# Kernel tuning notes

Hardware: AMD Instinct MI355X
Metric: run time of the kernel (lower is better)

The kernel has to match this reference:

```python
import jax, jax.numpy as jnp
import numpy as np

N_NODES = 10000


def gcn_conv(x, W, b, src, dst, n):
    # GCNConv (PyG defaults): linear transform, add self-loops, symmetric norm,
    # scatter-add aggregation at target nodes, then bias.
    h = x @ W  # [n, out]
    # degree with self-loops: 1 (self) + count of incoming edges per target node
    deg = jnp.ones((n,), h.dtype).at[dst].add(1.0)
    dinv = jax.lax.rsqrt(deg)  # deg >= 1 always
    norm = dinv[src] * dinv[dst]  # [E]
    # edge messages + self-loop contribution (norm_ii = dinv_i^2)
    agg = jnp.zeros_like(h).at[dst].add(h[src] * norm[:, None])
    agg = agg + h * (dinv * dinv)[:, None]
    return agg + b


def setup_inputs() -> dict:
    key = jax.random.key(0)
    ks = jax.random.split(key, 8)
    d_in, d_hid, d_out = 512, 512, 100
    n, e = N_NODES, 160000
    x = jax.random.normal(ks[0], (n, d_in), dtype=jnp.float32)
    edge_index = jax.random.randint(ks[1], (2, e), 0, n, dtype=jnp.int64)
    s1 = 1.0 / np.sqrt(d_in)
    s2 = 1.0 / np.sqrt(d_hid)
    W1 = jax.random.uniform(ks[2], (d_in, d_hid), jnp.float32, -s1, s1)
    b1 = jnp.zeros((d_hid,), jnp.float32)
    W2 = jax.random.uniform(ks[3], (d_hid, d_hid), jnp.float32, -s2, s2)
    b2 = jnp.zeros((d_hid,), jnp.float32)
    Wc = jax.random.uniform(ks[4], (d_hid, d_out), jnp.float32, -s2, s2)
    bc = jax.random.uniform(ks[5], (d_out,), jnp.float32, -s2, s2)
    return {"x": x, "edge_index": edge_index, "W1": W1, "b1": b1,
            "W2": W2, "b2": b2, "Wc": Wc, "bc": bc}


def reference(x, edge_index, W1, b1, W2, b2, Wc, bc):
    src, dst = edge_index[0], edge_index[1]
    n = x.shape[0]
    h = gcn_conv(x, W1, b1, src, dst, n)
    h = jax.nn.relu(h)  # dropout is identity in eval mode
    h = gcn_conv(h, W2, b2, src, dst, n)
    return h @ Wc + bc
```

## Files before the change

### kernel.cpp

```cpp
#include <hip/hip_runtime.h>
#include <hip/hip_bf16.h>
#include <stdint.h>

typedef __bf16 bf16_t;
typedef bf16_t bf16x8 __attribute__((ext_vector_type(8)));
typedef float f32x4 __attribute__((ext_vector_type(4)));

#define NN 10000
#define ELLCAP 64

__device__ __forceinline__ float b2f(unsigned short u) {
  union { unsigned int i; float f; } c; c.i = ((unsigned int)u) << 16; return c.f;
}
__device__ __forceinline__ unsigned short f2b(float f) {
  union { float f; unsigned int i; } c; c.f = f;
  unsigned int x = c.i;
  x += 0x7FFFu + ((x >> 16) & 1u);
  return (unsigned short)(x >> 16);
}
__device__ __forceinline__ uint4 cvt8(float4 a, float4 b) {
  uint4 r;
  r.x = (unsigned int)f2b(a.x) | ((unsigned int)f2b(a.y) << 16);
  r.y = (unsigned int)f2b(a.z) | ((unsigned int)f2b(a.w) << 16);
  r.z = (unsigned int)f2b(b.x) | ((unsigned int)f2b(b.y) << 16);
  r.w = (unsigned int)f2b(b.z) | ((unsigned int)f2b(b.w) << 16);
  return r;
}
__device__ __forceinline__ void load_lds16(const void* g, void* l) {
  __builtin_amdgcn_global_load_lds(
      (const __attribute__((address_space(1))) unsigned int*)g,
      (__attribute__((address_space(3))) unsigned int*)l, 16, 0, 0);
}
__device__ __forceinline__ f32x4 mfma16(bf16x8 a, bf16x8 b, f32x4 c) {
  return __builtin_amdgcn_mfma_f32_16x16x32_bf16(a, b, c, 0, 0, 0);
}

template <bool OBF16>
__device__ void gemm64(const unsigned short* __restrict__ A, const unsigned short* __restrict__ Bt,
                       void* __restrict__ Cv, int M, int Ncols, int ldc, int tm, int tn,
                       unsigned short* __restrict__ As, unsigned short* __restrict__ Bs)
{
  const int tid = threadIdx.x;
  const int lane = tid & 63;
  const int wn = tid >> 6;
  const int quad = lane >> 4, l15 = lane & 15;

  const int r0 = tid >> 2, kc = tid & 3;
  int ga = tm * 64 + r0;  if (ga > M - 1) ga = M - 1;
  const int gb0 = tn * 128 + r0;
  const int gb1 = tn * 128 + 64 + r0;
  const unsigned short* gA  = A + (size_t)ga * 512 + kc * 8;
  const unsigned short* gB0 = Bt + (size_t)gb0 * 512 + kc * 8;
  const unsigned short* gB1 = Bt + (size_t)gb1 * 512 + kc * 8;
  const int loff  = r0 * 32 + kc * 8;
  const int loff1 = (64 + r0) * 32 + kc * 8;
  const int ABUF = 64 * 32, BBUF = 128 * 32;

  f32x4 acc[4][2];
  #pragma unroll
  for (int i = 0; i < 4; i++)
    #pragma unroll
    for (int j = 0; j < 2; j++) {
      f32x4 z = {0.f, 0.f, 0.f, 0.f};
      acc[i][j] = z;
    }

  load_lds16(gA,  &As[loff]);
  load_lds16(gB0, &Bs[loff]);
  load_lds16(gB1, &Bs[loff1]);
  __syncthreads();

  for (int it = 0; it < 16; ++it) {
    const int ca = (it & 1) * ABUF, cb = (it & 1) * BBUF;
    if (it < 15) {
      const int k1 = (it + 1) * 32;
      const int na = ((it & 1) ^ 1) * ABUF, nb = ((it & 1) ^ 1) * BBUF;
      load_lds16(gA + k1,  &As[na + loff]);
      load_lds16(gB0 + k1, &Bs[nb + loff]);
      load_lds16(gB1 + k1, &Bs[nb + loff1]);
    }
    bf16x8 af[4], bfr[2];
    #pragma unroll
    for (int i = 0; i < 4; i++)
      af[i] = *(const bf16x8*)&As[ca + (i * 16 + l15) * 32 + quad * 8];
    #pragma unroll
    for (int j = 0; j < 2; j++)
      bfr[j] = *(const bf16x8*)&Bs[cb + (wn * 32 + j * 16 + l15) * 32 + quad * 8];
    #pragma unroll
    for (int i = 0; i < 4; i++)
      #pragma unroll
      for (int j = 0; j < 2; j++)
        acc[i][j] = mfma16(af[i], bfr[j], acc[i][j]);
    __syncthreads();
  }

  #pragma unroll
  for (int i = 0; i < 4; i++) {
    const int row_base = tm * 64 + i * 16 + quad * 4;
    #pragma unroll
    for (int j = 0; j < 2; j++) {
      const int col = tn * 128 + wn * 32 + j * 16 + l15;
      if (col < Ncols) {
        #pragma unroll
        for (int r = 0; r < 4; r++) {
          int row = row_base + r;
          if (row < M) {
            float v = acc[i][j][r];
            if (OBF16) ((unsigned short*)Cv)[(size_t)row * ldc + col] = f2b(v);
            else       ((float*)Cv)[(size_t)row * ldc + col] = v;
          }
        }
      }
    }
  }
}

__device__ void gemm64_f32A(const float* __restrict__ A, const unsigned short* __restrict__ Bt,
                            unsigned short* __restrict__ C, int M, int tm, int tn,
                            unsigned short* __restrict__ As, unsigned short* __restrict__ Bs)
{
  const int tid = threadIdx.x;
  const int lane = tid & 63;
  const int wn = tid >> 6;
  const int quad = lane >> 4, l15 = lane & 15;

  const int r0 = tid >> 2, kc = tid & 3;
  int ga = tm * 64 + r0;  if (ga > M - 1) ga = M - 1;
  const int gb0 = tn * 128 + r0;
  const int gb1 = tn * 128 + 64 + r0;
  const float* gA = A + (size_t)ga * 512 + kc * 8;
  const unsigned short* gB0 = Bt + (size_t)gb0 * 512 + kc * 8;
  const unsigned short* gB1 = Bt + (size_t)gb1 * 512 + kc * 8;
  const int loff  = r0 * 32 + kc * 8;
  const int loff1 = (64 + r0) * 32 + kc * 8;
  const int ABUF = 64 * 32, BBUF = 128 * 32;

  f32x4 acc[4][2];
  #pragma unroll
  for (int i = 0; i < 4; i++)
    #pragma unroll
    for (int j = 0; j < 2; j++) {
      f32x4 z = {0.f, 0.f, 0.f, 0.f};
      acc[i][j] = z;
    }

  {
    float4 a0 = *(const float4*)(gA), a1 = *(const float4*)(gA + 4);
    *(uint4*)&As[loff] = cvt8(a0, a1);
    load_lds16(gB0, &Bs[loff]);
    load_lds16(gB1, &Bs[loff1]);
  }
  __syncthreads();

  for (int it = 0; it < 16; ++it) {
    const int ca = (it & 1) * ABUF, cb = (it & 1) * BBUF;
    const int na = ((it & 1) ^ 1) * ABUF, nb = ((it & 1) ^ 1) * BBUF;
    float4 a0, a1;
    if (it < 15) {
      const int k1 = (it + 1) * 32;
      a0 = *(const float4*)(gA + k1);  a1 = *(const float4*)(gA + k1 + 4);
      load_lds16(gB0 + k1, &Bs[nb + loff]);
      load_lds16(gB1 + k1, &Bs[nb + loff1]);
    }
    bf16x8 af[4], bfr[2];
    #pragma unroll
    for (int i = 0; i < 4; i++)
      af[i] = *(const bf16x8*)&As[ca + (i * 16 + l15) * 32 + quad * 8];
    #pragma unroll
    for (int j = 0; j < 2; j++)
      bfr[j] = *(const bf16x8*)&Bs[cb + (wn * 32 + j * 16 + l15) * 32 + quad * 8];
    #pragma unroll
    for (int i = 0; i < 4; i++)
      #pragma unroll
      for (int j = 0; j < 2; j++)
        acc[i][j] = mfma16(af[i], bfr[j], acc[i][j]);
    if (it < 15) *(uint4*)&As[na + loff] = cvt8(a0, a1);
    __syncthreads();
  }

  #pragma unroll
  for (int i = 0; i < 4; i++) {
    const int row_base = tm * 64 + i * 16 + quad * 4;
    #pragma unroll
    for (int j = 0; j < 2; j++) {
      const int col = tn * 128 + wn * 32 + j * 16 + l15;
      #pragma unroll
      for (int r = 0; r < 4; r++) {
        int row = row_base + r;
        if (row < M) C[(size_t)row * 512 + col] = f2b(acc[i][j][r]);
      }
    }
  }
}

__device__ void wtrans_tile(const float* __restrict__ W, unsigned short* __restrict__ Wt,
                            int ncols, int tr0, int tc0)
{
  __shared__ float tile[64][65];
  const int t = threadIdx.x;
  const int r = t >> 2, c4 = t & 3;
  #pragma unroll
  for (int i = 0; i < 4; i++) {
    int col = c4 * 16 + i * 4;
    int gc = tc0 + col;
    float4 v;
    if (gc + 3 < ncols) {
      v = *(const float4*)&W[(size_t)(tr0 + r) * ncols + gc];
    } else {
      v.x = (gc + 0 < ncols) ? W[(size_t)(tr0 + r) * ncols + gc + 0] : 0.f;
      v.y = (gc + 1 < ncols) ? W[(size_t)(tr0 + r) * ncols + gc + 1] : 0.f;
      v.z = (gc + 2 < ncols) ? W[(size_t)(tr0 + r) * ncols + gc + 2] : 0.f;
      v.w = (gc + 3 < ncols) ? W[(size_t)(tr0 + r) * ncols + gc + 3] : 0.f;
    }
    tile[r][col] = v.x; tile[r][col + 1] = v.y;
    tile[r][col + 2] = v.z; tile[r][col + 3] = v.w;
  }
  __syncthreads();
  const int o = t >> 2;
  #pragma unroll
  for (int i = 0; i < 4; i++) {
    int k = c4 * 16 + i * 4;
    ushort4 u;
    u.x = f2b(tile[k + 0][o]); u.y = f2b(tile[k + 1][o]);
    u.z = f2b(tile[k + 2][o]); u.w = f2b(tile[k + 3][o]);
    *(ushort4*)&Wt[(size_t)(tc0 + o) * 512 + tr0 + k] = u;
  }
}

__global__ __launch_bounds__(256)
void prep_fill(const float* __restrict__ W1, const float* __restrict__ Wc,
               const float* __restrict__ W2, const int* __restrict__ src,
               const int* __restrict__ dst, int* __restrict__ cnt,
               int* __restrict__ ell, unsigned short* __restrict__ W1t,
               unsigned short* __restrict__ Wct, unsigned short* __restrict__ w2b, int E)
{
  if (blockIdx.x < 64) { wtrans_tile(W1, W1t, 512, (blockIdx.x >> 3) * 64, (blockIdx.x & 7) * 64); return; }
  if (blockIdx.x < 80) { int b = blockIdx.x - 64; wtrans_tile(Wc, Wct, 100, (b >> 1) * 64, (b & 1) * 64); return; }
  const int t0 = (blockIdx.x - 80) * 256 + threadIdx.x;
  const int FT = 160 * 256;
  const float4* W24 = (const float4*)W2;
  uint4* w2b4 = (uint4*)w2b;
  for (int i = t0; i < 512 * 512 / 8; i += FT)
    w2b4[i] = cvt8(W24[i * 2], W24[i * 2 + 1]);
  for (int e = t0; e < E; e += FT) {
    int s = src[e], d = dst[e];
    int pos = atomicAdd(&cnt[d], 1);
    if (pos < ELLCAP) ell[d * ELLCAP + pos] = s;
  }
}

__global__ __launch_bounds__(256)
void gemm1_fold(const float* __restrict__ x, const unsigned short* __restrict__ W1t,
                unsigned short* __restrict__ B2,
                const unsigned short* __restrict__ Wct, const unsigned short* __restrict__ w2b,
                unsigned short* __restrict__ W2WcT,
                const float* __restrict__ b2, const float* __restrict__ Wc,
                const float* __restrict__ bc, float* __restrict__ bias2c)
{
  __shared__ __align__(16) unsigned short As[2 * 64 * 32];
  __shared__ __align__(16) unsigned short Bs[2 * 128 * 32];
  const int b = blockIdx.x;
  if (b < 628) {
    gemm64_f32A(x, W1t, B2, NN, b >> 2, b & 3, As, Bs);
  } else if (b < 636) {
    const int g = b - 628;
    gemm64<true>(Wct, w2b, W2WcT, 128, 512, 512, g >> 2, g & 3, As, Bs);
  } else {
    const int j = threadIdx.x;
    if (j < 128) {
      float s = 0.f;
      if (j < 100) {
        s = bc[j];
        for (int k = 0; k < 512; k++) s = fmaf(b2[k], Wc[k * 100 + j], s);
      }
      bias2c[j] = s;
    }
  }
}

__device__ __forceinline__ void acc8(float* a, uint4 v, float nm) {
  a[0] = fmaf(b2f((unsigned short)(v.x & 0xffffu)), nm, a[0]);
  a[1] = fmaf(b2f((unsigned short)(v.x >> 16)),     nm, a[1]);
  a[2] = fmaf(b2f((unsigned short)(v.y & 0xffffu)), nm, a[2]);
  a[3] = fmaf(b2f((unsigned short)(v.y >> 16)),     nm, a[3]);
  a[4] = fmaf(b2f((unsigned short)(v.z & 0xffffu)), nm, a[4]);
  a[5] = fmaf(b2f((unsigned short)(v.z >> 16)),     nm, a[5]);
  a[6] = fmaf(b2f((unsigned short)(v.w & 0xffffu)), nm, a[6]);
  a[7] = fmaf(b2f((unsigned short)(v.w >> 16)),     nm, a[7]);
}

__global__ __launch_bounds__(256)
void gather1(const unsigned short* __restrict__ h, const int* __restrict__ cnt,
             const int* __restrict__ ell, const float* __restrict__ bias,
             unsigned short* __restrict__ outb, int n)
{
  int node = blockIdx.x * 4 + (threadIdx.x >> 6);
  if (node >= n) return;
  const int lane = threadIdx.x & 63;
  const int c8 = lane * 8;

  int cd = cnt[node]; if (cd > ELLCAP) cd = ELLCAP;
  const float fd = (float)(1 + cd);
  const float slf = 1.0f / fd;
  uint4 hv = *(const uint4*)&h[(size_t)node * 512 + c8];
  const float4* bp = (const float4*)&bias[c8];
  float4 b0 = bp[0], b1 = bp[1];
  float a[8] = {b0.x, b0.y, b0.z, b0.w, b1.x, b1.y, b1.z, b1.w};
  acc8(a, hv, slf);

  const int* row = ell + node * ELLCAP;
  int j = 0;
  for (; j + 8 <= cd; j += 8) {
    int ss[8]; uint4 vv[8]; float nm[8];
    #pragma unroll
    for (int q = 0; q < 8; q++) ss[q] = row[j + q];
    #pragma unroll
    for (int q = 0; q < 8; q++) vv[q] = *(const uint4*)&h[(size_t)ss[q] * 512 + c8];
    #pragma unroll
    for (int q = 0; q < 8; q++) nm[q] = rsqrtf((float)(1 + cnt[ss[q]]) * fd);
    #pragma unroll
    for (int q = 0; q < 8; q++) acc8(a, vv[q], nm[q]);
  }
  for (; j < cd; ++j) {
    int s = row[j];
    uint4 v = *(const uint4*)&h[(size_t)s * 512 + c8];
    acc8(a, v, rsqrtf((float)(1 + cnt[s]) * fd));
  }
  #pragma unroll
  for (int q = 0; q < 8; q++) a[q] = fmaxf(a[q], 0.f);
  uint4 o;
  o.x = (unsigned int)f2b(a[0]) | ((unsigned int)f2b(a[1]) << 16);
  o.y = (unsigned int)f2b(a[2]) | ((unsigned int)f2b(a[3]) << 16);
  o.z = (unsigned int)f2b(a[4]) | ((unsigned int)f2b(a[5]) << 16);
  o.w = (unsigned int)f2b(a[6]) | ((unsigned int)f2b(a[7]) << 16);
  *(uint4*)&outb[(size_t)node * 512 + c8] = o;
}

__global__ __launch_bounds__(256)
void gemm2c(const unsigned short* __restrict__ B1, const unsigned short* __restrict__ W2WcT,
            unsigned short* __restrict__ Z)
{
  __shared__ __align__(16) unsigned short As[2 * 64 * 32];
  __shared__ __align__(16) unsigned short Bs[2 * 128 * 32];
  gemm64<true>(B1, W2WcT, Z, NN, 128, 128, blockIdx.x, 0, As, Bs);
}

__global__ __launch_bounds__(256)
void gather2c(const unsigned short* __restrict__ Z, const int* __restrict__ cnt,
              const int* __restrict__ ell, const float* __restrict__ bias2c,
              float* __restrict__ out, int n)
{
  int node = blockIdx.x * 4 + (threadIdx.x >> 6);
  if (node >= n) return;
  const int lane = threadIdx.x & 63;
  const int c2 = lane * 2;
  const float2 bb = *(const float2*)&bias2c[c2];

  int cd = cnt[node]; if (cd > ELLCAP) cd = ELLCAP;
  const float fd = (float)(1 + cd);
  const float slf = 1.0f / fd;
  unsigned int hv = *(const unsigned int*)&Z[(size_t)node * 128 + c2];
  float a0 = fmaf(b2f((unsigned short)(hv & 0xffffu)), slf, bb.x);
  float a1 = fmaf(b2f((unsigned short)(hv >> 16)),     slf, bb.y);

  const int* row = ell + node * ELLCAP;
  int j = 0;
  for (; j + 8 <= cd; j += 8) {
    int ss[8]; unsigned int vv[8]; float nm[8];
    #pragma unroll
    for (int q = 0; q < 8; q++) ss[q] = row[j + q];
    #pragma unroll
    for (int q = 0; q < 8; q++) vv[q] = *(const unsigned int*)&Z[(size_t)ss[q] * 128 + c2];
    #pragma unroll
    for (int q = 0; q < 8; q++) nm[q] = rsqrtf((float)(1 + cnt[ss[q]]) * fd);
    #pragma unroll
    for (int q = 0; q < 8; q++) {
      a0 = fmaf(b2f((unsigned short)(vv[q] & 0xffffu)), nm[q], a0);
      a1 = fmaf(b2f((unsigned short)(vv[q] >> 16)),     nm[q], a1);
    }
  }
  for (; j < cd; ++j) {
    int s = row[j];
    unsigned int v = *(const unsigned int*)&Z[(size_t)s * 128 + c2];
    float nm = rsqrtf((float)(1 + cnt[s]) * fd);
    a0 = fmaf(b2f((unsigned short)(v & 0xffffu)), nm, a0);
    a1 = fmaf(b2f((unsigned short)(v >> 16)),     nm, a1);
  }
  if (c2 < 100)
    *(float2*)&out[(size_t)node * 100 + c2] = make_float2(a0, a1);
}

extern "C" void kernel_launch(void* const* d_in, const int* in_sizes, int n_in,
                              void* d_out, int out_size, void* d_ws, size_t ws_size,
                              hipStream_t stream) {
  const float* x  = (const float*)d_in[0];
  const int*   ei = (const int*)d_in[1];
  const float* W1 = (const float*)d_in[2];
  const float* b1 = (const float*)d_in[3];
  const float* W2 = (const float*)d_in[4];
  const float* b2 = (const float*)d_in[5];
  const float* Wc = (const float*)d_in[6];
  const float* bc = (const float*)d_in[7];
  float* out = (float*)d_out;

  const int n = NN;
  const int E = in_sizes[1] / 2;
  const int* src = ei;
  const int* dst = ei + E;

  char* w = (char*)d_ws;
  int* cnt = (int*)w;                       w += ((n * 4 + 255) / 256) * 256;
  int* ell = (int*)w;                       w += ((n * ELLCAP * 4 + 255) / 256) * 256;
  float* bias2c = (float*)w;                w += 512;
  unsigned short* W1t = (unsigned short*)w; w += 512 * 512 * 2;
  unsigned short* Wct = (unsigned short*)w; w += 128 * 512 * 2;
  unsigned short* w2b = (unsigned short*)w; w += 512 * 512 * 2;
  unsigned short* W2WcT = (unsigned short*)w; w += 128 * 512 * 2;
  unsigned short* B1  = (unsigned short*)w; w += (size_t)n * 512 * 2;
  unsigned short* B2  = (unsigned short*)w; w += (size_t)n * 512 * 2;
  unsigned short* Z   = (unsigned short*)w; w += (size_t)n * 128 * 2;

  const int nb_g = (n + 3) / 4;

  hipMemsetAsync(cnt, 0, n * sizeof(int), stream);
  prep_fill<<<240, 256, 0, stream>>>(W1, Wc, W2, src, dst, cnt, ell, W1t, Wct, w2b, E);
  gemm1_fold<<<637, 256, 0, stream>>>(x, W1t, B2, Wct, w2b, W2WcT, b2, Wc, bc, bias2c);
  gather1<<<nb_g, 256, 0, stream>>>(B2, cnt, ell, b1, B1, n);
  gemm2c<<<157, 256, 0, stream>>>(B1, W2WcT, Z);
  gather2c<<<nb_g, 256, 0, stream>>>(Z, cnt, ell, bias2c, out, n);
}
```

Measured before the change: 157.4 us.

## Fold source-side degree norm into GEMM epilogues and pre-convert x to bf16

The GEMM epilogues now scale each output row by rsqrt(1+deg), so the gathers only sum neighbour rows and apply the destination dinv and bias at the end. This removes the per-edge cnt lookups and rsqrt calls from both gather kernels. Separately, x is converted to bf16 in prep_fill (stored in the B1 buffer), so the first GEMM uses the plain bf16 path with global-to-LDS loads. The cost is an extra full pass that writes x as bf16, and the first GEMM now depends on cnt being complete before it runs.

Measured after the change: 159.1 us. About the same (+1.1%).

```diff
diff --git a/kernel.cpp b/kernel.cpp
--- a/kernel.cpp
+++ b/kernel.cpp
@@ -35,9 +35,10 @@
   return __builtin_amdgcn_mfma_f32_16x16x32_bf16(a, b, c, 0, 0, 0);
 }
 
-template <bool OBF16>
+template <bool SCALED>
 __device__ void gemm64(const unsigned short* __restrict__ A, const unsigned short* __restrict__ Bt,
-                       void* __restrict__ Cv, int M, int Ncols, int ldc, int tm, int tn,
+                       unsigned short* __restrict__ C, const int* __restrict__ cntp,
+                       int M, int Ncols, int ldc, int tm, int tn,
                        unsigned short* __restrict__ As, unsigned short* __restrict__ Bs)
 {
   const int tid = threadIdx.x;
@@ -96,98 +97,21 @@
 
   #pragma unroll
   for (int i = 0; i < 4; i++) {
-    const int row_base = tm * 64 + i * 16 + quad * 4;
-    #pragma unroll
-    for (int j = 0; j < 2; j++) {
-      const int col = tn * 128 + wn * 32 + j * 16 + l15;
-      if (col < Ncols) {
+    #pragma unroll
+    for (int r = 0; r < 4; r++) {
+      const int row = tm * 64 + i * 16 + quad * 4 + r;
+      if (row < M) {
+        float dv = 1.f;
+        if (SCALED) {
+          int c = cntp[row]; if (c > ELLCAP) c = ELLCAP;
+          dv = rsqrtf((float)(1 + c));
+        }
         #pragma unroll
-        for (int r = 0; r < 4; r++) {
-          int row = row_base + r;
-          if (row < M) {
-            float v = acc[i][j][r];
-            if (OBF16) ((unsigned short*)Cv)[(size_t)row * ldc + col] = f2b(v);
-            else       ((float*)Cv)[(size_t)row * ldc + col] = v;
-          }
+        for (int j = 0; j < 2; j++) {
+          const int col = tn * 128 + wn * 32 + j * 16 + l15;
+          if (col < Ncols)
+            C[(size_t)row * ldc + col] = f2b(acc[i][j][r] * dv);
         }
-      }
-    }
-  }
-}
-
-__device__ void gemm64_f32A(const float* __restrict__ A, const unsigned short* __restrict__ Bt,
-                            unsigned short* __restrict__ C, int M, int tm, int tn,
-                            unsigned short* __restrict__ As, unsigned short* __restrict__ Bs)
-{
-  const int tid = threadIdx.x;
-  const int lane = tid & 63;
-  const int wn = tid >> 6;
-  const int quad = lane >> 4, l15 = lane & 15;
-
-  const int r0 = tid >> 2, kc = tid & 3;
-  int ga = tm * 64 + r0;  if (ga > M - 1) ga = M - 1;
-  const int gb0 = tn * 128 + r0;
-  const int gb1 = tn * 128 + 64 + r0;
-  const float* gA = A + (size_t)ga * 512 + kc * 8;
-  const unsigned short* gB0 = Bt + (size_t)gb0 * 512 + kc * 8;
-  const unsigned short* gB1 = Bt + (size_t)gb1 * 512 + kc * 8;
-  const int loff  = r0 * 32 + kc * 8;
-  const int loff1 = (64 + r0) * 32 + kc * 8;
-  const int ABUF = 64 * 32, BBUF = 128 * 32;
-
-  f32x4 acc[4][2];
-  #pragma unroll
-  for (int i = 0; i < 4; i++)
-    #pragma unroll
-    for (int j = 0; j < 2; j++) {
-      f32x4 z = {0.f, 0.f, 0.f, 0.f};
-      acc[i][j] = z;
-    }
-
-  {
-    float4 a0 = *(const float4*)(gA), a1 = *(const float4*)(gA + 4);
-    *(uint4*)&As[loff] = cvt8(a0, a1);
-    load_lds16(gB0, &Bs[loff]);
-    load_lds16(gB1, &Bs[loff1]);
-  }
-  __syncthreads();
-
-  for (int it = 0; it < 16; ++it) {
-    const int ca = (it & 1) * ABUF, cb = (it & 1) * BBUF;
-    const int na = ((it & 1) ^ 1) * ABUF, nb = ((it & 1) ^ 1) * BBUF;
-    float4 a0, a1;
-    if (it < 15) {
-      const int k1 = (it + 1) * 32;
-      a0 = *(const float4*)(gA + k1);  a1 = *(const float4*)(gA + k1 + 4);
-      load_lds16(gB0 + k1, &Bs[nb + loff]);
-      load_lds16(gB1 + k1, &Bs[nb + loff1]);
-    }
-    bf16x8 af[4], bfr[2];
-    #pragma unroll
-    for (int i = 0; i < 4; i++)
-      af[i] = *(const bf16x8*)&As[ca + (i * 16 + l15) * 32 + quad * 8];
-    #pragma unroll
-    for (int j = 0; j < 2; j++)
-      bfr[j] = *(const bf16x8*)&Bs[cb + (wn * 32 + j * 16 + l15) * 32 + quad * 8];
-    #pragma unroll
-    for (int i = 0; i < 4; i++)
-      #pragma unroll
-      for (int j = 0; j < 2; j++)
-        acc[i][j] = mfma16(af[i], bfr[j], acc[i][j]);
-    if (it < 15) *(uint4*)&As[na + loff] = cvt8(a0, a1);
-    __syncthreads();
-  }
-
-  #pragma unroll
-  for (int i = 0; i < 4; i++) {
-    const int row_base = tm * 64 + i * 16 + quad * 4;
-    #pragma unroll
-    for (int j = 0; j < 2; j++) {
-      const int col = tn * 128 + wn * 32 + j * 16 + l15;
-      #pragma unroll
-      for (int r = 0; r < 4; r++) {
-        int row = row_base + r;
-        if (row < M) C[(size_t)row * 512 + col] = f2b(acc[i][j][r]);
       }
     }
   }
@@ -229,19 +153,24 @@
 
 __global__ __launch_bounds__(256)
 void prep_fill(const float* __restrict__ W1, const float* __restrict__ Wc,
-               const float* __restrict__ W2, const int* __restrict__ src,
-               const int* __restrict__ dst, int* __restrict__ cnt,
-               int* __restrict__ ell, unsigned short* __restrict__ W1t,
-               unsigned short* __restrict__ Wct, unsigned short* __restrict__ w2b, int E)
+               const float* __restrict__ W2, const float* __restrict__ x,
+               const int* __restrict__ src, const int* __restrict__ dst,
+               int* __restrict__ cnt, int* __restrict__ ell,
+               unsigned short* __restrict__ W1t, unsigned short* __restrict__ Wct,
+               unsigned short* __restrict__ w2b, unsigned short* __restrict__ xb, int E)
 {
   if (blockIdx.x < 64) { wtrans_tile(W1, W1t, 512, (blockIdx.x >> 3) * 64, (blockIdx.x & 7) * 64); return; }
   if (blockIdx.x < 80) { int b = blockIdx.x - 64; wtrans_tile(Wc, Wct, 100, (b >> 1) * 64, (b & 1) * 64); return; }
   const int t0 = (blockIdx.x - 80) * 256 + threadIdx.x;
-  const int FT = 160 * 256;
+  const int FT = 256 * 256;
   const float4* W24 = (const float4*)W2;
   uint4* w2b4 = (uint4*)w2b;
   for (int i = t0; i < 512 * 512 / 8; i += FT)
     w2b4[i] = cvt8(W24[i * 2], W24[i * 2 + 1]);
+  const float4* x4 = (const float4*)x;
+  uint4* xb4 = (uint4*)xb;
+  for (int i = t0; i < NN * 512 / 8; i += FT)
+    xb4[i] = cvt8(x4[i * 2], x4[i * 2 + 1]);
   for (int e = t0; e < E; e += FT) {
     int s = src[e], d = dst[e];
     int pos = atomicAdd(&cnt[d], 1);
@@ -250,8 +179,8 @@
 }
 
 __global__ __launch_bounds__(256)
-void gemm1_fold(const float* __restrict__ x, const unsigned short* __restrict__ W1t,
-                unsigned short* __restrict__ B2,
+void gemm1_fold(const unsigned short* __restrict__ xb, const unsigned short* __restrict__ W1t,
+                unsigned short* __restrict__ B2, const int* __restrict__ cnt,
                 const unsigned short* __restrict__ Wct, const unsigned short* __restrict__ w2b,
                 unsigned short* __restrict__ W2WcT,
                 const float* __restrict__ b2, const float* __restrict__ Wc,
@@ -261,10 +190,10 @@
   __shared__ __align__(16) unsigned short Bs[2 * 128 * 32];
   const int b = blockIdx.x;
   if (b < 628) {
-    gemm64_f32A(x, W1t, B2, NN, b >> 2, b & 3, As, Bs);
+    gemm64<true>(xb, W1t, B2, cnt, NN, 512, 512, b >> 2, b & 3, As, Bs);
   } else if (b < 636) {
     const int g = b - 628;
-    gemm64<true>(Wct, w2b, W2WcT, 128, 512, 512, g >> 2, g & 3, As, Bs);
+    gemm64<false>(Wct, w2b, W2WcT, nullptr, 128, 512, 512, g >> 2, g & 3, As, Bs);
   } else {
     const int j = threadIdx.x;
     if (j < 128) {
@@ -278,15 +207,15 @@
   }
 }
 
-__device__ __forceinline__ void acc8(float* a, uint4 v, float nm) {
-  a[0] = fmaf(b2f((unsigned short)(v.x & 0xffffu)), nm, a[0]);
-  a[1] = fmaf(b2f((unsigned short)(v.x >> 16)),     nm, a[1]);
-  a[2] = fmaf(b2f((unsigned short)(v.y & 0xffffu)), nm, a[2]);
-  a[3] = fmaf(b2f((unsigned short)(v.y >> 16)),     nm, a[3]);
-  a[4] = fmaf(b2f((unsigned short)(v.z & 0xffffu)), nm, a[4]);
-  a[5] = fmaf(b2f((unsigned short)(v.z >> 16)),     nm, a[5]);
-  a[6] = fmaf(b2f((unsigned short)(v.w & 0xffffu)), nm, a[6]);
-  a[7] = fmaf(b2f((unsigned short)(v.w >> 16)),     nm, a[7]);
+__device__ __forceinline__ void add8(float* a, uint4 v) {
+  a[0] += b2f((unsigned short)(v.x & 0xffffu));
+  a[1] += b2f((unsigned short)(v.x >> 16));
+  a[2] += b2f((unsigned short)(v.y & 0xffffu));
+  a[3] += b2f((unsigned short)(v.y >> 16));
+  a[4] += b2f((unsigned short)(v.z & 0xffffu));
+  a[5] += b2f((unsigned short)(v.z >> 16));
+  a[6] += b2f((unsigned short)(v.w & 0xffffu));
+  a[7] += b2f((unsigned short)(v.w >> 16));
 }
 
 __global__ __launch_bounds__(256)
@@ -300,34 +229,33 @@
   const int c8 = lane * 8;
 
   int cd = cnt[node]; if (cd > ELLCAP) cd = ELLCAP;
-  const float fd = (float)(1 + cd);
-  const float slf = 1.0f / fd;
+  const float dinv = rsqrtf((float)(1 + cd));
   uint4 hv = *(const uint4*)&h[(size_t)node * 512 + c8];
-  const float4* bp = (const float4*)&bias[c8];
-  float4 b0 = bp[0], b1 = bp[1];
-  float a[8] = {b0.x, b0.y, b0.z, b0.w, b1.x, b1.y, b1.z, b1.w};
-  acc8(a, hv, slf);
+  float a[8] = {0.f, 0.f, 0.f, 0.f, 0.f, 0.f, 0.f, 0.f};
+  add8(a, hv);
 
   const int* row = ell + node * ELLCAP;
   int j = 0;
   for (; j + 8 <= cd; j += 8) {
-    int ss[8]; uint4 vv[8]; float nm[8];
+    int ss[8]; uint4 vv[8];
     #pragma unroll
     for (int q = 0; q < 8; q++) ss[q] = row[j + q];
     #pragma unroll
     for (int q = 0; q < 8; q++) vv[q] = *(const uint4*)&h[(size_t)ss[q] * 512 + c8];
     #pragma unroll
-    for (int q = 0; q < 8; q++) nm[q] = rsqrtf((float)(1 + cnt[ss[q]]) * fd);
-    #pragma unroll
-    for (int q = 0; q < 8; q++) acc8(a, vv[q], nm[q]);
+    for (int q = 0; q < 8; q++) add8(a, vv[q]);
   }
   for (; j < cd; ++j) {
     int s = row[j];
     uint4 v = *(const uint4*)&h[(size_t)s * 512 + c8];
-    acc8(a, v, rsqrtf((float)(1 + cnt[s]) * fd));
-  }
-  #pragma unroll
-  for (int q = 0; q < 8; q++) a[q] = fmaxf(a[q], 0.f);
+    add8(a, v);
+  }
+
+  const float4* bp = (const float4*)&bias[c8];
+  float4 b0 = bp[0], b1 = bp[1];
+  float bb[8] = {b0.x, b0.y, b0.z, b0.w, b1.x, b1.y, b1.z, b1.w};
+  #pragma unroll
+  for (int q = 0; q < 8; q++) a[q] = fmaxf(fmaf(a[q], dinv, bb[q]), 0.f);
   uint4 o;
   o.x = (unsigned int)f2b(a[0]) | ((unsigned int)f2b(a[1]) << 16);
   o.y = (unsigned int)f2b(a[2]) | ((unsigned int)f2b(a[3]) << 16);
@@ -338,11 +266,11 @@
 
 __global__ __launch_bounds__(256)
 void gemm2c(const unsigned short* __restrict__ B1, const unsigned short* __restrict__ W2WcT,
-            unsigned short* __restrict__ Z)
+            unsigned short* __restrict__ Z, const int* __restrict__ cnt)
 {
   __shared__ __align__(16) unsigned short As[2 * 64 * 32];
   __shared__ __align__(16) unsigned short Bs[2 * 128 * 32];
-  gemm64<true>(B1, W2WcT, Z, NN, 128, 128, blockIdx.x, 0, As, Bs);
+  gemm64<true>(B1, W2WcT, Z, cnt, NN, 128, 128, blockIdx.x, 0, As, Bs);
 }
 
 __global__ __launch_bounds__(256)
@@ -354,40 +282,38 @@
   if (node >= n) return;
   const int lane = threadIdx.x & 63;
   const int c2 = lane * 2;
-  const float2 bb = *(const float2*)&bias2c[c2];
 
   int cd = cnt[node]; if (cd > ELLCAP) cd = ELLCAP;
-  const float fd = (float)(1 + cd);
-  const float slf = 1.0f / fd;
+  const float dinv = rsqrtf((float)(1 + cd));
   unsigned int hv = *(const unsigned int*)&Z[(size_t)node * 128 + c2];
-  float a0 = fmaf(b2f((unsigned short)(hv & 0xffffu)), slf, bb.x);
-  float a1 = fmaf(b2f((unsigned short)(hv >> 16)),     slf, bb.y);
+  float a0 = b2f((unsigned short)(hv & 0xffffu));
+  float a1 = b2f((unsigned short)(hv >> 16));
 
   const int* row = ell + node * ELLCAP;
   int j = 0;
   for (; j + 8 <= cd; j += 8) {
-    int ss[8]; unsigned int vv[8]; float nm[8];
+    int ss[8]; unsigned int vv[8];
     #pragma unroll
     for (int q = 0; q < 8; q++) ss[q] = row[j + q];
     #pragma unroll
     for (int q = 0; q < 8; q++) vv[q] = *(const unsigned int*)&Z[(size_t)ss[q] * 128 + c2];
     #pragma unroll
-    for (int q = 0; q < 8; q++) nm[q] = rsqrtf((float)(1 + cnt[ss[q]]) * fd);
-    #pragma unroll
     for (int q = 0; q < 8; q++) {
-      a0 = fmaf(b2f((unsigned short)(vv[q] & 0xffffu)), nm[q], a0);
-      a1 = fmaf(b2f((unsigned short)(vv[q] >> 16)),     nm[q], a1);
+      a0 += b2f((unsigned short)(vv[q] & 0xffffu));
+      a1 += b2f((unsigned short)(vv[q] >> 16));
     }
   }
   for (; j < cd; ++j) {
     int s = row[j];
     unsigned int v = *(const unsigned int*)&Z[(size_t)s * 128 + c2];
-    float nm = rsqrtf((float)(1 + cnt[s]) * fd);
-    a0 = fmaf(b2f((unsigned short)(v & 0xffffu)), nm, a0);
-    a1 = fmaf(b2f((unsigned short)(v >> 16)),     nm, a1);
-  }
-  if (c2 < 100)
-    *(float2*)&out[(size_t)node * 100 + c2] = make_float2(a0, a1);
+    a0 += b2f((unsigned short)(v & 0xffffu));
+    a1 += b2f((unsigned short)(v >> 16));
+  }
+  if (c2 < 100) {
+    const float2 bb = *(const float2*)&bias2c[c2];
+    *(float2*)&out[(size_t)node * 100 + c2] =
+        make_float2(fmaf(a0, dinv, bb.x), fmaf(a1, dinv, bb.y));
+  }
 }
 
 extern "C" void kernel_launch(void* const* d_in, const int* in_sizes, int n_in,
@@ -420,12 +346,14 @@
   unsigned short* B2  = (unsigned short*)w; w += (size_t)n * 512 * 2;
   unsigned short* Z   = (unsigned short*)w; w += (size_t)n * 128 * 2;
 
+  unsigned short* xb = B1;
+
   const int nb_g = (n + 3) / 4;
 
   hipMemsetAsync(cnt, 0, n * sizeof(int), stream);
-  prep_fill<<<240, 256, 0, stream>>>(W1, Wc, W2, src, dst, cnt, ell, W1t, Wct, w2b, E);
-  gemm1_fold<<<637, 256, 0, stream>>>(x, W1t, B2, Wct, w2b, W2WcT, b2, Wc, bc, bias2c);
+  prep_fill<<<336, 256, 0, stream>>>(W1, Wc, W2, x, src, dst, cnt, ell, W1t, Wct, w2b, xb, E);
+  gemm1_fold<<<637, 256, 0, stream>>>(xb, W1t, B2, cnt, Wct, w2b, W2WcT, b2, Wc, bc, bias2c);
   gather1<<<nb_g, 256, 0, stream>>>(B2, cnt, ell, b1, B1, n);
-  gemm2c<<<157, 256, 0, stream>>>(B1, W2WcT, Z);
+  gemm2c<<<157, 256, 0, stream>>>(B1, W2WcT, Z, cnt);
   gather2c<<<nb_g, 256, 0, stream>>>(Z, cnt, ell, bias2c, out, n);
 }
```
